# Kernel optimization log

Measured on AMD Instinct MI355X. Metric: run time of the kernel, lower is better.

The kernel has to match this reference:

```python
import jax, jax.numpy as jnp
import numpy as np

SIGMA = 10
POPULATIONS = 2
LR = 0.001


def _normalize(L, prior):
    # clamp then normalize over populations (logsumexp across the population axis)
    O = L.shape[1]
    L = jnp.clip(L, -5.0, 0.0)
    lse = jax.nn.logsumexp(L.reshape(POPULATIONS, -1, O), axis=0)  # (in/P, O)
    L = L - jnp.tile(lse, (POPULATIONS, 1))
    prior = jnp.clip(prior, -5.0, 0.0)
    prior = prior - jax.nn.logsumexp(prior)
    return L, prior


def _forward(x, L, prior):
    B, T, IN = x.shape
    O = L.shape[1]
    L, prior = _normalize(L, prior)  # matches normalize_probs() in __init__

    # membrane potential: OR of spikes over trailing window of SIGMA steps
    xb = x.astype(bool)
    pot = xb
    for s in range(1, SIGMA):  # fixed small loop (sigma=10)
        pot = pot | jnp.pad(xb, ((0, 0), (s, 0), (0, 0)))[:, :T, :]

    tpre0 = jnp.full((B, IN), -T, dtype=jnp.int32)
    tpost0 = jnp.full((B, O), jnp.iinfo(jnp.int32).max, dtype=jnp.int32)
    base_key = jax.random.key(42)

    pot_T = jnp.transpose(pot, (1, 0, 2))  # (T,B,IN)
    x_T = jnp.transpose(xb, (1, 0, 2))

    def step(carry, inp):
        L, prior, tpre, tpost, t = carry
        pot_t, x_t = inp
        potf = pot_t.astype(L.dtype)
        logits = potf @ L + prior  # (B,O), logits <= 0 so exp is safe
        # torch: softmax(exp(logits)).multinomial == categorical with logits=exp(logits)
        key = jax.random.fold_in(base_key, t)
        widx = jax.random.categorical(key, jnp.exp(logits), axis=-1)  # (B,)
        win = jax.nn.one_hot(widx, O, dtype=L.dtype)
        # trace updates happen BEFORE STDP, as in the torch code
        tpre = jnp.where(x_t, 0, tpre - 1)
        tpost = jnp.where(win > 0, 0, tpost - 1)
        ltp = (tpre >= -SIGMA).astype(L.dtype)
        ltd = (tpre < -SIGMA).astype(L.dtype)
        post = (tpost < 0).astype(L.dtype)
        m_ltp = jnp.einsum('bi,bo->io', ltp, win) / B
        m_ltd = jnp.einsum('bi,bo->io', ltd, win) / B
        m_pp = jnp.einsum('bi,bo->io', potf, post) / B
        decay = (t + 1).astype(L.dtype)  # lr_decay_inverse starts at 1
        # dw = (5 e^{-L} - 1) * LTP.mean - LTD.mean - pre_post.mean ; LTD was negated
        dw = (5.0 * jnp.exp(-L) - 1.0) * m_ltp + m_ltd - m_pp
        L2 = L + (LR / decay) * dw
        wm = jnp.mean(win, axis=0)
        db = (-5.0 * prior - 1.0) * wm - (1.0 - wm)
        p2 = prior + (LR / decay) * db
        L2, p2 = _normalize(L2, p2)
        return (L2, p2, tpre, tpost, t + 1), None

    (Lf, pf, _, _, _), _ = jax.lax.scan(
        step, (L, prior, tpre0, tpost0, jnp.int32(0)), (pot_T, x_T))
    return jnp.concatenate([Lf.reshape(-1), pf])


def setup_inputs() -> dict:
    key = jax.random.key(0)
    k1, k2, k3 = jax.random.split(key, 3)
    B, T, IN, O = 256, 200, 1568, 100
    x = jax.random.randint(k1, (B, T, IN), 0, 2, dtype=jnp.int32)
    log_likelihood = jax.random.uniform(k2, (IN, O), dtype=jnp.float32) * -1.0 - 1.0
    log_prior = jax.random.uniform(k3, (O,), dtype=jnp.float32) * -1.0 - 1.0
    return {"x": x, "log_likelihood": log_likelihood, "log_prior": log_prior}


def reference(x, log_likelihood, log_prior):
    return _forward(x, log_likelihood, log_prior)
```

## Files before the change

kernel.cpp:

```cpp
#include <hip/hip_runtime.h>
#include <stdint.h>

#define BB 256
#define TT 200
#define INN 1568
#define OO 100
#define PAIRS 784
#define NHALF 12800

typedef unsigned long long u64;
typedef __attribute__((ext_vector_type(4))) int v4i;

__device__ __forceinline__ void tf_round(uint32_t& x0, uint32_t& x1, int r) {
    x0 += x1;
    x1 = (x1 << r) | (x1 >> (32 - r));
    x1 ^= x0;
}

__device__ __forceinline__ void threefry(uint32_t k0, uint32_t k1,
                                         uint32_t x0, uint32_t x1,
                                         uint32_t& o0, uint32_t& o1) {
    uint32_t k2 = k0 ^ k1 ^ 0x1BD11BDAu;
    x0 += k0; x1 += k1;
    tf_round(x0,x1,13); tf_round(x0,x1,15); tf_round(x0,x1,26); tf_round(x0,x1,6);
    x0 += k1; x1 += k2 + 1u;
    tf_round(x0,x1,17); tf_round(x0,x1,29); tf_round(x0,x1,16); tf_round(x0,x1,24);
    x0 += k2; x1 += k0 + 2u;
    tf_round(x0,x1,13); tf_round(x0,x1,15); tf_round(x0,x1,26); tf_round(x0,x1,6);
    x0 += k0; x1 += k1 + 3u;
    tf_round(x0,x1,17); tf_round(x0,x1,29); tf_round(x0,x1,16); tf_round(x0,x1,24);
    x0 += k1; x1 += k2 + 4u;
    tf_round(x0,x1,13); tf_round(x0,x1,15); tf_round(x0,x1,26); tf_round(x0,x1,6);
    o0 = x0 + k2; o1 = x1 + k0 + 5u;
}

__global__ __launch_bounds__(64) void k_winbit(const int* __restrict__ x,
                                               uint8_t* __restrict__ widx,
                                               u64* __restrict__ bitB) {
    if (blockIdx.x < 800) {
        int idx = blockIdx.x * 64 + threadIdx.x;
        int t = idx >> 8, b = idx & 255;
        uint32_t fk0, fk1;
        threefry(0u, 42u, 0u, (uint32_t)t, fk0, fk1);
        uint32_t bestkey = 0u;
        int bo = 0;
        int nbase = b * OO;
        for (int o = 0; o < OO; ++o) {
            uint32_t n = (uint32_t)(nbase + o);
            uint32_t lo = (n < NHALF) ? n : n - NHALF;
            uint32_t v0, v1;
            threefry(fk0, fk1, lo, lo + NHALF, v0, v1);
            uint32_t bits = (n < NHALF) ? v0 : v1;
            uint32_t key = bits >> 9;
            if (key > bestkey) { bestkey = key; bo = o; }
        }
        widx[idx] = (uint8_t)bo;
    } else {
        int idx = (blockIdx.x - 800) * 64 + threadIdx.x;
        int wb = idx / (TT * 392);
        int r = idx - wb * (TT * 392);
        int t = r / 392;
        int ig = r - t * 392;
        const v4i* xp = (const v4i*)x;
        u64 m0 = 0, m1 = 0, m2 = 0, m3 = 0;
        for (int j = 0; j < 64; ++j) {
            int b = wb * 64 + j;
            v4i v = __builtin_nontemporal_load(&xp[((size_t)b * TT + t) * 392 + ig]);
            u64 bit = 1ull << j;
            if (v.x) m0 |= bit;
            if (v.y) m1 |= bit;
            if (v.z) m2 |= bit;
            if (v.w) m3 |= bit;
        }
        u64* dst = bitB + ((size_t)(t * 4 + wb)) * INN + 4 * ig;
        dst[0] = m0; dst[1] = m1; dst[2] = m2; dst[3] = m3;
    }
}

__global__ __launch_bounds__(256) void k_fwpost(const uint8_t* __restrict__ widx,
                                                u64* __restrict__ winbits,
                                                u64* __restrict__ postbits,
                                                uint32_t* __restrict__ cnt) {
    __shared__ uint32_t wl32[TT * 65];
    __shared__ int fwl[BB];
    int o = blockIdx.x;
    int tid = threadIdx.x;
    const uint32_t* wsrc = (const uint32_t*)widx;
    for (int g = tid; g < TT * 64; g += 256) {
        int t = g >> 6, w = g & 63;
        wl32[t * 65 + w] = wsrc[g];
    }
    __syncthreads();
    if (tid < 64) {
        int f0 = 255, f1 = 255, f2 = 255, f3 = 255;
        for (int t = 0; t < TT; ++t) {
            uint32_t w4 = wl32[t * 65 + tid];
            if (((w4      ) & 255u) == (uint32_t)o && f0 == 255) f0 = t;
            if (((w4 >>  8) & 255u) == (uint32_t)o && f1 == 255) f1 = t;
            if (((w4 >> 16) & 255u) == (uint32_t)o && f2 == 255) f2 = t;
            if (((w4 >> 24) & 255u) == (uint32_t)o && f3 == 255) f3 = t;
        }
        fwl[4 * tid + 0] = f0; fwl[4 * tid + 1] = f1;
        fwl[4 * tid + 2] = f2; fwl[4 * tid + 3] = f3;
    }
    __syncthreads();
    if (tid < TT) {
        int t = tid;
        u64 wbA[4], pbA[4];
        uint32_t c = 0;
        #pragma unroll
        for (int k = 0; k < 4; ++k) {
            u64 wacc = 0, pacc = 0;
            for (int q2 = 0; q2 < 16; ++q2) {
                uint32_t w4 = wl32[t * 65 + k * 16 + q2];
                #pragma unroll
                for (int j = 0; j < 4; ++j) {
                    int bl = q2 * 4 + j;
                    bool win = (((w4 >> (8 * j)) & 255u) == (uint32_t)o);
                    c += win ? 1u : 0u;
                    bool post = (fwl[k * 64 + q2 * 4 + j] < t) && !win;
                    u64 bit = 1ull << bl;
                    if (win)  wacc |= bit;
                    if (post) pacc |= bit;
                }
            }
            wbA[k] = wacc; pbA[k] = pacc;
        }
        size_t base = (size_t)(t * OO + o) * 4;
        #pragma unroll
        for (int k = 0; k < 4; ++k) {
            winbits[base + k] = wbA[k];
            postbits[base + k] = pbA[k];
        }
        cnt[t * OO + o] = c;
    }
}

__global__ __launch_bounds__(64) void k_popcW(
        const u64* __restrict__ bitB,
        const u64* __restrict__ winbits,
        const u64* __restrict__ postbits,
        uint32_t* __restrict__ packed,
        int t0) {
    __shared__ u64 winS[OO * 4];
    __shared__ u64 postS[OO * 4];
    int tl = blockIdx.y;
    int t = t0 + tl;
    int tid = threadIdx.x;
    for (int idx = tid; idx < OO * 4; idx += 64) {
        winS[idx]  = winbits[(size_t)t * OO * 4 + idx];
        postS[idx] = postbits[(size_t)t * OO * 4 + idx];
    }
    __syncthreads();
    int p = blockIdx.x * 64 + tid;
    if (p >= PAIRS) return;
    int i0 = p, i1 = p + PAIRS;
    u64 p0=0,p1=0,p2=0,p3=0,p4=0,p5=0,p6=0,p7=0;
    int ttlo = (t - 9 < 0) ? 0 : t - 9;
    for (int tt = ttlo; tt <= t; ++tt) {
        const u64* row = bitB + (size_t)tt * 4 * INN;
        p0 |= row[i0];           p1 |= row[INN + i0];
        p2 |= row[2 * INN + i0]; p3 |= row[3 * INN + i0];
        p4 |= row[i1];           p5 |= row[INN + i1];
        p6 |= row[2 * INN + i1]; p7 |= row[3 * INN + i1];
    }
    u64 l0=p0,l1=p1,l2=p2,l3=p3,l4=p4,l5=p5,l6=p6,l7=p7;
    if (t >= 10) {
        const u64* row = bitB + (size_t)(t - 10) * 4 * INN;
        l0 |= row[i0];           l1 |= row[INN + i0];
        l2 |= row[2 * INN + i0]; l3 |= row[3 * INN + i0];
        l4 |= row[i1];           l5 |= row[INN + i1];
        l6 |= row[2 * INN + i1]; l7 |= row[3 * INN + i1];
    }
    uint32_t* orow = packed + (size_t)tl * OO * PAIRS + p;
    #pragma unroll 4
    for (int o = 0; o < OO; ++o) {
        const u64* w = &winS[o * 4];
        const u64* s = &postS[o * 4];
        uint32_t lt0 = __popcll(l0 & w[0]) + __popcll(l1 & w[1])
                     + __popcll(l2 & w[2]) + __popcll(l3 & w[3]);
        uint32_t lt1 = __popcll(l4 & w[0]) + __popcll(l5 & w[1])
                     + __popcll(l6 & w[2]) + __popcll(l7 & w[3]);
        uint32_t pp0 = __popcll(p0 & s[0]) + __popcll(p1 & s[1])
                     + __popcll(p2 & s[2]) + __popcll(p3 & s[3]);
        uint32_t pp1 = __popcll(p4 & s[0]) + __popcll(p5 & s[1])
                     + __popcll(p6 & s[2]) + __popcll(p7 & s[3]);
        lt0 = (lt0 > 255u) ? 255u : lt0;  pp0 = (pp0 > 255u) ? 255u : pp0;
        lt1 = (lt1 > 255u) ? 255u : lt1;  pp1 = (pp1 > 255u) ? 255u : pp1;
        uint32_t v = lt0 | (pp0 << 8) | (lt1 << 16) | (pp1 << 24);
        __builtin_nontemporal_store(v, &orow[(size_t)o * PAIRS]);
    }
}

__global__ __launch_bounds__(64) void k_chainsPrior(
        const float* __restrict__ L0,
        const float* __restrict__ p0arr,
        const uint32_t* __restrict__ packed,
        const uint32_t* __restrict__ cnt,
        float* __restrict__ outL,
        float* __restrict__ outp,
        int t0, int ct, int first, int do_prior) {
    if (blockIdx.y == OO) {
        if (!do_prior || blockIdx.x != 0) return;
        int l = threadIdx.x;
        bool has2 = (l + 64) < OO;
        float pa = p0arr[l];
        float pb = has2 ? p0arr[l + 64] : -1e30f;
        auto normalize = [&]() {
            pa = fminf(fmaxf(pa, -5.0f), 0.0f);
            if (has2) pb = fminf(fmaxf(pb, -5.0f), 0.0f);
            float mx = has2 ? fmaxf(pa, pb) : pa;
            #pragma unroll
            for (int s = 32; s > 0; s >>= 1) mx = fmaxf(mx, __shfl_xor(mx, s, 64));
            float sm = expf(pa - mx) + (has2 ? expf(pb - mx) : 0.0f);
            #pragma unroll
            for (int s = 32; s > 0; s >>= 1) sm += __shfl_xor(sm, s, 64);
            float lse = logf(sm) + mx;
            pa -= lse;
            if (has2) pb -= lse;
        };
        normalize();
        for (int t = 0; t < TT; ++t) {
            float eta = 0.001f / (float)(t + 1);
            float wma = (float)cnt[t * OO + l] * (1.0f / 256.0f);
            pa += eta * ((-5.0f * pa - 1.0f) * wma - (1.0f - wma));
            if (has2) {
                float wmb = (float)cnt[t * OO + l + 64] * (1.0f / 256.0f);
                pb += eta * ((-5.0f * pb - 1.0f) * wmb - (1.0f - wmb));
            }
            normalize();
        }
        outp[l] = pa;
        if (has2) outp[l + 64] = pb;
        return;
    }
    int o = blockIdx.y;
    int p = blockIdx.x * 64 + threadIdx.x;
    if (p >= PAIRS) return;
    int i0 = p, i1 = p + PAIRS;
    float a, b2;
    if (first) {
        a  = L0[(size_t)i0 * OO + o];
        b2 = L0[(size_t)i1 * OO + o];
        a  = fminf(fmaxf(a,  -5.0f), 0.0f);
        b2 = fminf(fmaxf(b2, -5.0f), 0.0f);
        float m = fmaxf(a, b2), mn = fminf(a, b2);
        float lse = __logf(1.0f + __expf(mn - m)) + m;
        a -= lse; b2 -= lse;
    } else {
        a  = outL[(size_t)i0 * OO + o];
        b2 = outL[(size_t)i1 * OO + o];
    }
    const uint32_t* src = packed + (size_t)o * PAIRS + p;
    const size_t tstride = (size_t)OO * PAIRS;
    uint32_t c[16];
    #pragma unroll
    for (int k = 0; k < 16; ++k) {
        int idx = (k < ct) ? k : (ct - 1);
        c[k] = __builtin_nontemporal_load(&src[(size_t)idx * tstride]);
    }
    #pragma unroll 16
    for (int tl = 0; tl < ct; ++tl) {
        uint32_t cur = c[tl & 15];
        int nx = tl + 16; if (nx >= ct) nx = ct - 1;
        c[tl & 15] = __builtin_nontemporal_load(&src[(size_t)nx * tstride]);
        int t = t0 + tl;
        float cwin = (float)cnt[t * OO + o];
        float lt0 = (float)(cur & 255u),         pp0 = (float)((cur >> 8) & 255u);
        float lt1 = (float)((cur >> 16) & 255u), pp1 = (float)(cur >> 24);
        float eta = 0.001f / (float)(t + 1);
        float dw0 = (5.0f * __expf(-a)  - 1.0f) * (lt0 * (1.0f/256.0f))
                  + (cwin - lt0 - pp0) * (1.0f/256.0f);
        float dw1 = (5.0f * __expf(-b2) - 1.0f) * (lt1 * (1.0f/256.0f))
                  + (cwin - lt1 - pp1) * (1.0f/256.0f);
        a  += eta * dw0;
        b2 += eta * dw1;
        a  = fminf(fmaxf(a,  -5.0f), 0.0f);
        b2 = fminf(fmaxf(b2, -5.0f), 0.0f);
        float m = fmaxf(a, b2), mn = fminf(a, b2);
        float lse = __logf(1.0f + __expf(mn - m)) + m;
        a -= lse; b2 -= lse;
    }
    outL[(size_t)i0 * OO + o] = a;
    outL[(size_t)i1 * OO + o] = b2;
}

extern "C" void kernel_launch(void* const* d_in, const int* in_sizes, int n_in,
                              void* d_out, int out_size, void* d_ws, size_t ws_size,
                              hipStream_t stream) {
    const int*   x  = (const int*)d_in[0];
    const float* L0 = (const float*)d_in[1];
    const float* p0 = (const float*)d_in[2];
    float* out = (float*)d_out;

    char* ws = (char*)d_ws;
    size_t off = 0;
    auto alloc = [&](size_t bytes) -> void* {
        off = (off + 255) & ~(size_t)255;
        void* p = ws + off;
        off += bytes;
        return p;
    };
    uint8_t*  widx     = (uint8_t*) alloc((size_t)TT * BB);
    uint32_t* cnt      = (uint32_t*)alloc((size_t)TT * OO * 4);
    u64*      winbits  = (u64*)     alloc((size_t)TT * OO * 4 * 8);
    u64*      postbits = (u64*)     alloc((size_t)TT * OO * 4 * 8);
    u64*      bitB     = (u64*)     alloc((size_t)TT * 4 * INN * 8);

    static const int cands[] = {200, 100, 50, 25, 20, 10, 8, 5, 4, 2, 1};
    int CT = 1;
    size_t base_off = (off + 255) & ~(size_t)255;
    for (int c = 0; c < 11; ++c) {
        size_t need = base_off + (size_t)cands[c] * OO * PAIRS * 4;
        if (need <= ws_size) { CT = cands[c]; break; }
    }
    uint32_t* packed = (uint32_t*)(ws + base_off);

    hipLaunchKernelGGL(k_winbit, dim3(800 + 4900), dim3(64), 0, stream, x, widx, bitB);
    hipLaunchKernelGGL(k_fwpost, dim3(OO), dim3(256), 0, stream,
                       widx, winbits, postbits, cnt);
    for (int t0 = 0; t0 < TT; t0 += CT) {
        int ct = (t0 + CT <= TT) ? CT : (TT - t0);
        int last = (t0 + ct >= TT) ? 1 : 0;
        hipLaunchKernelGGL(k_popcW, dim3((PAIRS + 63) / 64, ct), dim3(64), 0, stream,
                           bitB, winbits, postbits, packed, t0);
        hipLaunchKernelGGL(k_chainsPrior, dim3((PAIRS + 63) / 64, OO + 1), dim3(64),
                           0, stream, L0, p0, packed, cnt, out,
                           out + (size_t)INN * OO, t0, ct, (t0 == 0) ? 1 : 0, last);
    }
}
```

Measured before the change: 632.3 us.

## Fuse popcount and per-weight update chains into one time-looping kernel

Replaces the two-kernel scheme, which wrote packed per-timestep popcount bytes to global memory and read them back, with a single fused kernel. Each block owns a 16-pair by 20-output tile and loops over all 200 timesteps. Spike-window bits, win and post masks and counts for the next step are double-buffered in shared memory and prefetched while the current step's update runs. This removes the large packed intermediate buffer and its global traffic, and drops the 8-bit saturation of counts. In exchange only 250 blocks are launched, each with a __syncthreads per step, so occupancy and latency hiding may be limited.

```diff
diff --git a/kernel.cpp b/kernel.cpp
--- a/kernel.cpp
+++ b/kernel.cpp
@@ -136,73 +136,24 @@
     }
 }
 
-__global__ __launch_bounds__(64) void k_popcW(
+#define PBLK 16
+#define OBLK 20
+#define FTHR 320
+#define ROWSTRIDE (4 * INN)
+
+__global__ __launch_bounds__(FTHR) void k_fused(
+        const float* __restrict__ L0,
+        const float* __restrict__ p0arr,
         const u64* __restrict__ bitB,
         const u64* __restrict__ winbits,
         const u64* __restrict__ postbits,
-        uint32_t* __restrict__ packed,
-        int t0) {
-    __shared__ u64 winS[OO * 4];
-    __shared__ u64 postS[OO * 4];
-    int tl = blockIdx.y;
-    int t = t0 + tl;
-    int tid = threadIdx.x;
-    for (int idx = tid; idx < OO * 4; idx += 64) {
-        winS[idx]  = winbits[(size_t)t * OO * 4 + idx];
-        postS[idx] = postbits[(size_t)t * OO * 4 + idx];
-    }
-    __syncthreads();
-    int p = blockIdx.x * 64 + tid;
-    if (p >= PAIRS) return;
-    int i0 = p, i1 = p + PAIRS;
-    u64 p0=0,p1=0,p2=0,p3=0,p4=0,p5=0,p6=0,p7=0;
-    int ttlo = (t - 9 < 0) ? 0 : t - 9;
-    for (int tt = ttlo; tt <= t; ++tt) {
-        const u64* row = bitB + (size_t)tt * 4 * INN;
-        p0 |= row[i0];           p1 |= row[INN + i0];
-        p2 |= row[2 * INN + i0]; p3 |= row[3 * INN + i0];
-        p4 |= row[i1];           p5 |= row[INN + i1];
-        p6 |= row[2 * INN + i1]; p7 |= row[3 * INN + i1];
-    }
-    u64 l0=p0,l1=p1,l2=p2,l3=p3,l4=p4,l5=p5,l6=p6,l7=p7;
-    if (t >= 10) {
-        const u64* row = bitB + (size_t)(t - 10) * 4 * INN;
-        l0 |= row[i0];           l1 |= row[INN + i0];
-        l2 |= row[2 * INN + i0]; l3 |= row[3 * INN + i0];
-        l4 |= row[i1];           l5 |= row[INN + i1];
-        l6 |= row[2 * INN + i1]; l7 |= row[3 * INN + i1];
-    }
-    uint32_t* orow = packed + (size_t)tl * OO * PAIRS + p;
-    #pragma unroll 4
-    for (int o = 0; o < OO; ++o) {
-        const u64* w = &winS[o * 4];
-        const u64* s = &postS[o * 4];
-        uint32_t lt0 = __popcll(l0 & w[0]) + __popcll(l1 & w[1])
-                     + __popcll(l2 & w[2]) + __popcll(l3 & w[3]);
-        uint32_t lt1 = __popcll(l4 & w[0]) + __popcll(l5 & w[1])
-                     + __popcll(l6 & w[2]) + __popcll(l7 & w[3]);
-        uint32_t pp0 = __popcll(p0 & s[0]) + __popcll(p1 & s[1])
-                     + __popcll(p2 & s[2]) + __popcll(p3 & s[3]);
-        uint32_t pp1 = __popcll(p4 & s[0]) + __popcll(p5 & s[1])
-                     + __popcll(p6 & s[2]) + __popcll(p7 & s[3]);
-        lt0 = (lt0 > 255u) ? 255u : lt0;  pp0 = (pp0 > 255u) ? 255u : pp0;
-        lt1 = (lt1 > 255u) ? 255u : lt1;  pp1 = (pp1 > 255u) ? 255u : pp1;
-        uint32_t v = lt0 | (pp0 << 8) | (lt1 << 16) | (pp1 << 24);
-        __builtin_nontemporal_store(v, &orow[(size_t)o * PAIRS]);
-    }
-}
-
-__global__ __launch_bounds__(64) void k_chainsPrior(
-        const float* __restrict__ L0,
-        const float* __restrict__ p0arr,
-        const uint32_t* __restrict__ packed,
         const uint32_t* __restrict__ cnt,
         float* __restrict__ outL,
-        float* __restrict__ outp,
-        int t0, int ct, int first, int do_prior) {
-    if (blockIdx.y == OO) {
-        if (!do_prior || blockIdx.x != 0) return;
+        float* __restrict__ outp) {
+    if (blockIdx.x == 49) {
+        if (blockIdx.y != 0) return;
         int l = threadIdx.x;
+        if (l >= 64) return;
         bool has2 = (l + 64) < OO;
         float pa = p0arr[l];
         float pb = has2 ? p0arr[l + 64] : -1e30f;
@@ -234,45 +185,98 @@
         if (has2) outp[l + 64] = pb;
         return;
     }
-    int o = blockIdx.y;
-    int p = blockIdx.x * 64 + threadIdx.x;
-    if (p >= PAIRS) return;
-    int i0 = p, i1 = p + PAIRS;
-    float a, b2;
-    if (first) {
-        a  = L0[(size_t)i0 * OO + o];
-        b2 = L0[(size_t)i1 * OO + o];
-        a  = fminf(fmaxf(a,  -5.0f), 0.0f);
-        b2 = fminf(fmaxf(b2, -5.0f), 0.0f);
+
+    __shared__ u64 potL[2][PBLK * 10];
+    __shared__ u64 ltpL[2][PBLK * 10];
+    __shared__ u64 winL[2][OBLK * 4];
+    __shared__ u64 postL[2][OBLK * 4];
+    __shared__ float cntL[2][OBLK];
+
+    int tid = threadIdx.x;
+    int p0 = blockIdx.x * PBLK;
+    int o0 = blockIdx.y * OBLK;
+    int pl = tid & 15;
+    int ol = tid >> 4;
+    int o  = o0 + ol;
+    int i0 = p0 + pl;
+    int i1 = i0 + PAIRS;
+
+    const u64* colbase = bitB + (size_t)(ol & 3) * INN
+                       + ((ol < 8) ? (size_t)(p0 + pl + (ol >> 2) * PAIRS) : 0);
+    int s  = tid - 128;
+    int ols = s >> 3, js = s & 7;
+
+    if (tid < 128) {
+        u64 acc = 0, r0 = 0;
+        #pragma unroll
+        for (int ii = 0; ii < 11; ++ii) {
+            int tt = ii - 10; tt = (tt < 0) ? 0 : tt;
+            u64 v = colbase[(size_t)tt * ROWSTRIDE];
+            if (ii == 0) r0 = v; else acc |= v;
+        }
+        potL[0][pl * 10 + ol] = acc;
+        ltpL[0][pl * 10 + ol] = acc | r0;
+    } else if (tid < 288) {
+        size_t base = (size_t)(o0 + ols) * 4;
+        if (js < 4) winL[0][ols * 4 + js] = winbits[base + js];
+        else        postL[0][ols * 4 + js - 4] = postbits[base + js - 4];
+    } else if (tid < 308) {
+        cntL[0][tid - 288] = (float)cnt[o0 + (tid - 288)];
+    }
+
+    float a  = L0[(size_t)i0 * OO + o];
+    float b2 = L0[(size_t)i1 * OO + o];
+    a  = fminf(fmaxf(a,  -5.0f), 0.0f);
+    b2 = fminf(fmaxf(b2, -5.0f), 0.0f);
+    {
         float m = fmaxf(a, b2), mn = fminf(a, b2);
         float lse = __logf(1.0f + __expf(mn - m)) + m;
         a -= lse; b2 -= lse;
-    } else {
-        a  = outL[(size_t)i0 * OO + o];
-        b2 = outL[(size_t)i1 * OO + o];
-    }
-    const uint32_t* src = packed + (size_t)o * PAIRS + p;
-    const size_t tstride = (size_t)OO * PAIRS;
-    uint32_t c[16];
-    #pragma unroll
-    for (int k = 0; k < 16; ++k) {
-        int idx = (k < ct) ? k : (ct - 1);
-        c[k] = __builtin_nontemporal_load(&src[(size_t)idx * tstride]);
-    }
-    #pragma unroll 16
-    for (int tl = 0; tl < ct; ++tl) {
-        uint32_t cur = c[tl & 15];
-        int nx = tl + 16; if (nx >= ct) nx = ct - 1;
-        c[tl & 15] = __builtin_nontemporal_load(&src[(size_t)nx * tstride]);
-        int t = t0 + tl;
-        float cwin = (float)cnt[t * OO + o];
-        float lt0 = (float)(cur & 255u),         pp0 = (float)((cur >> 8) & 255u);
-        float lt1 = (float)((cur >> 16) & 255u), pp1 = (float)(cur >> 24);
+    }
+    __syncthreads();
+
+    for (int t = 0; t < TT; ++t) {
+        int cur = t & 1, nxt = cur ^ 1;
+        bool pre = (t + 1 < TT);
+        u64 wv[11];
+        u64 stg = 0; float cstg = 0.0f;
+        if (pre) {
+            if (tid < 128) {
+                int tb = t + 1 - 10;
+                #pragma unroll
+                for (int ii = 0; ii < 11; ++ii) {
+                    int tt = tb + ii; tt = (tt < 0) ? 0 : tt;
+                    wv[ii] = colbase[(size_t)tt * ROWSTRIDE];
+                }
+            } else if (tid < 288) {
+                size_t base = (size_t)((t + 1) * OO + o0 + ols) * 4;
+                stg = (js < 4) ? winbits[base + js] : postbits[base + js - 4];
+            } else if (tid < 308) {
+                cstg = (float)cnt[(t + 1) * OO + o0 + (tid - 288)];
+            }
+        }
+        u64 W0 = winL[cur][ol * 4 + 0], W1 = winL[cur][ol * 4 + 1];
+        u64 W2 = winL[cur][ol * 4 + 2], W3 = winL[cur][ol * 4 + 3];
+        u64 S0 = postL[cur][ol * 4 + 0], S1 = postL[cur][ol * 4 + 1];
+        u64 S2 = postL[cur][ol * 4 + 2], S3 = postL[cur][ol * 4 + 3];
+        const u64* Pp = &potL[cur][pl * 10];
+        const u64* Lp = &ltpL[cur][pl * 10];
+        uint32_t lt0 = __popcll(Lp[0] & W0) + __popcll(Lp[1] & W1)
+                     + __popcll(Lp[2] & W2) + __popcll(Lp[3] & W3);
+        uint32_t lt1 = __popcll(Lp[4] & W0) + __popcll(Lp[5] & W1)
+                     + __popcll(Lp[6] & W2) + __popcll(Lp[7] & W3);
+        uint32_t pp0 = __popcll(Pp[0] & S0) + __popcll(Pp[1] & S1)
+                     + __popcll(Pp[2] & S2) + __popcll(Pp[3] & S3);
+        uint32_t pp1 = __popcll(Pp[4] & S0) + __popcll(Pp[5] & S1)
+                     + __popcll(Pp[6] & S2) + __popcll(Pp[7] & S3);
+        float cwin = cntL[cur][ol];
+        float lt0f = (float)lt0, lt1f = (float)lt1;
+        float pp0f = (float)pp0, pp1f = (float)pp1;
         float eta = 0.001f / (float)(t + 1);
-        float dw0 = (5.0f * __expf(-a)  - 1.0f) * (lt0 * (1.0f/256.0f))
-                  + (cwin - lt0 - pp0) * (1.0f/256.0f);
-        float dw1 = (5.0f * __expf(-b2) - 1.0f) * (lt1 * (1.0f/256.0f))
-                  + (cwin - lt1 - pp1) * (1.0f/256.0f);
+        float dw0 = (5.0f * __expf(-a)  - 1.0f) * (lt0f * (1.0f/256.0f))
+                  + (cwin - lt0f - pp0f) * (1.0f/256.0f);
+        float dw1 = (5.0f * __expf(-b2) - 1.0f) * (lt1f * (1.0f/256.0f))
+                  + (cwin - lt1f - pp1f) * (1.0f/256.0f);
         a  += eta * dw0;
         b2 += eta * dw1;
         a  = fminf(fmaxf(a,  -5.0f), 0.0f);
@@ -280,6 +284,20 @@
         float m = fmaxf(a, b2), mn = fminf(a, b2);
         float lse = __logf(1.0f + __expf(mn - m)) + m;
         a -= lse; b2 -= lse;
+        if (pre) {
+            if (tid < 128) {
+                u64 acc = wv[1] | wv[2] | wv[3] | wv[4] | wv[5]
+                        | wv[6] | wv[7] | wv[8] | wv[9] | wv[10];
+                potL[nxt][pl * 10 + ol] = acc;
+                ltpL[nxt][pl * 10 + ol] = acc | wv[0];
+            } else if (tid < 288) {
+                if (js < 4) winL[nxt][ols * 4 + js] = stg;
+                else        postL[nxt][ols * 4 + js - 4] = stg;
+            } else if (tid < 308) {
+                cntL[nxt][tid - 288] = cstg;
+            }
+        }
+        __syncthreads();
     }
     outL[(size_t)i0 * OO + o] = a;
     outL[(size_t)i1 * OO + o] = b2;
@@ -306,26 +324,12 @@
     u64*      winbits  = (u64*)     alloc((size_t)TT * OO * 4 * 8);
     u64*      postbits = (u64*)     alloc((size_t)TT * OO * 4 * 8);
     u64*      bitB     = (u64*)     alloc((size_t)TT * 4 * INN * 8);
-
-    static const int cands[] = {200, 100, 50, 25, 20, 10, 8, 5, 4, 2, 1};
-    int CT = 1;
-    size_t base_off = (off + 255) & ~(size_t)255;
-    for (int c = 0; c < 11; ++c) {
-        size_t need = base_off + (size_t)cands[c] * OO * PAIRS * 4;
-        if (need <= ws_size) { CT = cands[c]; break; }
-    }
-    uint32_t* packed = (uint32_t*)(ws + base_off);
+    (void)ws_size;
 
     hipLaunchKernelGGL(k_winbit, dim3(800 + 4900), dim3(64), 0, stream, x, widx, bitB);
     hipLaunchKernelGGL(k_fwpost, dim3(OO), dim3(256), 0, stream,
                        widx, winbits, postbits, cnt);
-    for (int t0 = 0; t0 < TT; t0 += CT) {
-        int ct = (t0 + CT <= TT) ? CT : (TT - t0);
-        int last = (t0 + ct >= TT) ? 1 : 0;
-        hipLaunchKernelGGL(k_popcW, dim3((PAIRS + 63) / 64, ct), dim3(64), 0, stream,
-                           bitB, winbits, postbits, packed, t0);
-        hipLaunchKernelGGL(k_chainsPrior, dim3((PAIRS + 63) / 64, OO + 1), dim3(64),
-                           0, stream, L0, p0, packed, cnt, out,
-                           out + (size_t)INN * OO, t0, ct, (t0 == 0) ? 1 : 0, last);
-    }
-}
+    hipLaunchKernelGGL(k_fused, dim3(50, 5), dim3(FTHR), 0, stream,
+                       L0, p0, bitB, winbits, postbits, cnt,
+                       out, out + (size_t)INN * OO);
+}
```

New measurement: 617.4 us. 2.4% less time.
